# Performance work log

Hardware: AMD Instinct MI355X
Metric: run time of the kernel (lower is better)

## Reference

```python
import jax, jax.numpy as jnp
import numpy as np

EPS = 1e-05


def reference(inputs, c1, h1, c2, h2, w, b, norm_w, norm_b):
    B = inputs.shape[0]
    U = inputs.shape[1]
    # [B, 3U] @ [3U, 5U] + [1, 5U]
    x = jnp.concatenate([inputs, h1, h2], axis=1)
    res = x @ w + b
    # split into 5 contiguous gates -> [B, 5, U], layer-norm each gate over last axis
    g = res.reshape(B, 5, U)
    m = jnp.mean(g, axis=-1, keepdims=True)
    v = jnp.var(g, axis=-1, keepdims=True)  # biased variance, matches tf.nn.moments
    ln = (g - m) / jnp.sqrt(v + EPS) * norm_w[None, :, :] + norm_b[None, :, :]
    i, j, f, f2, o = ln[:, 0], ln[:, 1], ln[:, 2], ln[:, 3], ln[:, 4]
    new_c = c1 * jax.nn.sigmoid(f) + c2 * jax.nn.sigmoid(f2) + jax.nn.sigmoid(i) * jnp.tanh(j)
    new_h = new_c * jax.nn.sigmoid(o)
    return new_c, new_h


def setup_inputs() -> dict:
    B, U = 16384, 512
    key = jax.random.key(0)
    ks = jax.random.split(key, 6)
    return {
        "inputs": jax.random.normal(ks[0], (B, U), dtype=jnp.float32),
        "c1": jax.random.normal(ks[1], (B, U), dtype=jnp.float32),
        "h1": jax.random.normal(ks[2], (B, U), dtype=jnp.float32),
        "c2": jax.random.normal(ks[3], (B, U), dtype=jnp.float32),
        "h2": jax.random.normal(ks[4], (B, U), dtype=jnp.float32),
        "w": jax.random.normal(ks[5], (3 * U, 5 * U), dtype=jnp.float32) * (1.0 / np.sqrt(3 * U)),
        "b": jnp.zeros((1, 5 * U), dtype=jnp.float32),
        "norm_w": jnp.ones((5, U), dtype=jnp.float32),
        "norm_b": jnp.zeros((5, U), dtype=jnp.float32),
    }
```

## Files before the change

kernel.cpp:

```cpp
#include <hip/hip_runtime.h>
#include <hip/hip_bf16.h>
#include <cstdint>

#define B_DIM 16384
#define U_DIM 512
#define K_DIM 1536
#define N_DIM 2560
#define NT    24

typedef unsigned short u16;
typedef __attribute__((ext_vector_type(4))) unsigned short u16x4;
typedef __attribute__((ext_vector_type(8))) unsigned short u16x8;
typedef __attribute__((ext_vector_type(8))) short bf16x8;
typedef __attribute__((ext_vector_type(4))) float f32x4;

__device__ __forceinline__ u16 f2bf(float f) {
    uint32_t u = __builtin_bit_cast(uint32_t, f);
    u += 0x7FFFu + ((u >> 16) & 1u);
    return (u16)(u >> 16);
}
__device__ __forceinline__ float bf2f(u16 h) {
    uint32_t u = ((uint32_t)h) << 16;
    return __builtin_bit_cast(float, u);
}

__global__ void __launch_bounds__(256) cvt_x_kernel(
    const float* __restrict__ inp, const float* __restrict__ h1,
    const float* __restrict__ h2, u16* __restrict__ xb)
{
    int idx = blockIdx.x * 256 + threadIdx.x;
    const int total4 = B_DIM * K_DIM / 4;
    if (idx >= total4) return;
    int e = idx * 4;
    int b = e / K_DIM;
    int k = e - b * K_DIM;
    const float* src;
    if (k < 512)       src = inp + b * 512 + k;
    else if (k < 1024) src = h1  + b * 512 + (k - 512);
    else               src = h2  + b * 512 + (k - 1024);
    float4 v = *(const float4*)src;
    u16x4 o;
    o.x = f2bf(v.x); o.y = f2bf(v.y); o.z = f2bf(v.z); o.w = f2bf(v.w);
    *(u16x4*)(xb + e) = o;
}

__global__ void __launch_bounds__(256) cvt_wT_kernel(
    const float* __restrict__ w, u16* __restrict__ wT)
{
    __shared__ float tile[32][33];
    const int n0 = blockIdx.x * 32;
    const int k0 = blockIdx.y * 32;
    const int tx = threadIdx.x & 31;
    const int ty = threadIdx.x >> 5;
#pragma unroll
    for (int i = 0; i < 4; ++i) {
        int kk = ty + i * 8;
        tile[kk][tx] = w[(k0 + kk) * N_DIM + n0 + tx];
    }
    __syncthreads();
#pragma unroll
    for (int i = 0; i < 4; ++i) {
        int nn = ty + i * 8;
        wT[(int64_t)(n0 + nn) * K_DIM + k0 + tx] = f2bf(tile[tx][nn]);
    }
}

__device__ __forceinline__ void gload_lds16(const void* g, void* l) {
    __builtin_amdgcn_global_load_lds(
        (const __attribute__((address_space(1))) void*)g,
        (__attribute__((address_space(3))) void*)l, 16, 0, 0);
}

#define BAR    __builtin_amdgcn_s_barrier()
#define FENCE  asm volatile("" ::: "memory")
#define VMCNT3 asm volatile("s_waitcnt vmcnt(3)" ::: "memory")
#define LGKM0  do { asm volatile("s_waitcnt lgkmcnt(0)" ::: "memory"); \
                    __builtin_amdgcn_sched_barrier(0); } while (0)

__global__ void __launch_bounds__(512, 2) gemm_kernel(
    const u16* __restrict__ A, const u16* __restrict__ Bt,
    u16* __restrict__ C)
{
    __shared__ u16 sm[49152];

    const int tid  = threadIdx.x;
    const int lane = tid & 63;
    const int wave = tid >> 6;

    int bid = blockIdx.x;
    int swz = (bid & 7) * 160 + (bid >> 3);
    const int bm = (swz / 10) * 128;
    const int bn = (swz % 10) * 256;

    const int wm = (wave >> 2) * 64;
    const int wn = (wave & 3) * 64;

    const int l15 = lane & 15, cq = lane >> 4;
    const int s   = (((l15 & 1) << 2) | cq) ^ ((l15 >> 1) & 7);
    const int rdA = ((wm + l15) >> 1) * 64 + s * 8;
    const int rdB = ((wn + l15) >> 1) * 64 + s * 8;

    const int line0 = tid >> 3;
    const int rc    = (tid & 7) ^ (line0 & 7);
    const int srow  = line0 * 2 + (rc >> 2);
    const int sc8   = (rc & 3) * 8;
    const u16* gA = A  + (int64_t)(bm + srow) * K_DIM + sc8;
    const u16* gB = Bt + (int64_t)(bn + srow) * K_DIM + sc8;
    char* ldA = (char*)sm + tid * 16;
    char* ldB = (char*)sm + 16384 + tid * 16;

#define STAGE(ks, kt, buf) do {                                            \
        const u16* ga_ = gA + (kt) + (ks) * 32;                            \
        const u16* gb_ = gB + (kt) + (ks) * 32;                            \
        char* la_ = ldA + (buf) * 49152 + (ks) * 8192;                     \
        char* lb_ = ldB + (buf) * 49152 + (ks) * 16384;                    \
        gload_lds16(ga_, la_);                                             \
        gload_lds16(gb_, lb_);                                             \
        gload_lds16(gb_ + 128 * K_DIM, lb_ + 8192);                        \
    } while (0)

    f32x4 acc[4][4];
#pragma unroll
    for (int i = 0; i < 4; ++i)
#pragma unroll
        for (int j = 0; j < 4; ++j) acc[i][j] = (f32x4)(0.0f);

    STAGE(0, 0, 0);
    STAGE(1, 0, 0);
    VMCNT3;
    BAR; FENCE;

    bf16x8 af[4], bfr[4];

#define LOAD_A4(BASE) _Pragma("unroll")                                    \
    for (int mi = 0; mi < 4; ++mi) af[mi] = *(const bf16x8*)((BASE) + mi * 512)
#define LOAD_B4(BASE) _Pragma("unroll")                                    \
    for (int n = 0; n < 4; ++n) bfr[n] = *(const bf16x8*)((BASE) + n * 512)
#define MFMA16 _Pragma("unroll")                                           \
    for (int mi = 0; mi < 4; ++mi) { _Pragma("unroll")                     \
        for (int n = 0; n < 4; ++n)                                        \
            acc[mi][n] = __builtin_amdgcn_mfma_f32_16x16x32_bf16(          \
                af[mi], bfr[n], acc[mi][n], 0, 0, 0); }

    for (int t = 0; t < NT; ++t) {
        const int cur = t & 1, nxt = cur ^ 1;
        const int ktn = ((t + 1) == NT) ? 0 : (t + 1) * 64;
        const u16* base = sm + cur * 24576;

        LOAD_A4(base + rdA);
        LOAD_B4(base + 8192 + rdB);
        STAGE(0, ktn, nxt);
        BAR; LGKM0;
        __builtin_amdgcn_s_setprio(1);
        MFMA16;
        __builtin_amdgcn_s_setprio(0);
        VMCNT3;
        BAR; FENCE;

        LOAD_A4(base + 4096 + rdA);
        LOAD_B4(base + 8192 + 8192 + rdB);
        STAGE(1, ktn, nxt);
        BAR; LGKM0;
        __builtin_amdgcn_s_setprio(1);
        MFMA16;
        __builtin_amdgcn_s_setprio(0);
        VMCNT3;
        BAR; FENCE;
    }

    const int ecol = lane & 15;
    const int erow = (lane >> 4) * 4;
#pragma unroll
    for (int m = 0; m < 4; ++m)
#pragma unroll
        for (int n = 0; n < 4; ++n)
#pragma unroll
            for (int r = 0; r < 4; ++r) {
                int grow = bm + wm + m * 16 + erow + r;
                int gcol = bn + wn + n * 16 + ecol;
                C[(int64_t)grow * N_DIM + gcol] = f2bf(acc[m][n][r]);
            }
}

__device__ __forceinline__ float fsig(float x) {
    return 1.0f / (1.0f + __expf(-x));
}
__device__ __forceinline__ float ftanh(float x) {
    float e = __expf(-2.0f * fabsf(x));
    float r = (1.0f - e) / (1.0f + e);
    return copysignf(r, x);
}

__global__ void __launch_bounds__(256) ln_pointwise_kernel(
    const u16*  __restrict__ res,  const float* __restrict__ bias,
    const float* __restrict__ c1,  const float* __restrict__ c2,
    const float* __restrict__ nw,  const float* __restrict__ nb,
    float* __restrict__ out)
{
    const int wave = threadIdx.x >> 6;
    const int lane = threadIdx.x & 63;
    const int b    = blockIdx.x * 4 + wave;
    const u16* row = res + (int64_t)b * N_DIM;
    const int u0 = lane * 8;

    float v[5][8];
    float rstd[5], mean[5];

#pragma unroll
    for (int g = 0; g < 5; ++g) {
        u16x8 raw = *(const u16x8*)(row + g * 512 + u0);
        const float4* bp = (const float4*)(bias + g * 512 + u0);
        float4 b0 = bp[0], b1 = bp[1];
        v[g][0] = bf2f(raw[0]) + b0.x;  v[g][1] = bf2f(raw[1]) + b0.y;
        v[g][2] = bf2f(raw[2]) + b0.z;  v[g][3] = bf2f(raw[3]) + b0.w;
        v[g][4] = bf2f(raw[4]) + b1.x;  v[g][5] = bf2f(raw[5]) + b1.y;
        v[g][6] = bf2f(raw[6]) + b1.z;  v[g][7] = bf2f(raw[7]) + b1.w;
        float s = 0.f, q = 0.f;
#pragma unroll
        for (int j = 0; j < 8; ++j) { s += v[g][j]; q += v[g][j] * v[g][j]; }
#pragma unroll
        for (int off = 1; off < 64; off <<= 1) {
            s += __shfl_xor(s, off);
            q += __shfl_xor(q, off);
        }
        float m   = s * (1.0f / 512.0f);
        float var = q * (1.0f / 512.0f) - m * m;
        mean[g] = m;
        rstd[g] = rsqrtf(var + 1e-5f);
    }

#pragma unroll
    for (int g = 0; g < 5; ++g) {
        const float4* wp = (const float4*)(nw + g * 512 + u0);
        const float4* bp = (const float4*)(nb + g * 512 + u0);
        float4 w0 = wp[0], w1 = wp[1], n0 = bp[0], n1 = bp[1];
        float ws[8] = {w0.x, w0.y, w0.z, w0.w, w1.x, w1.y, w1.z, w1.w};
        float ns[8] = {n0.x, n0.y, n0.z, n0.w, n1.x, n1.y, n1.z, n1.w};
#pragma unroll
        for (int j = 0; j < 8; ++j)
            v[g][j] = (v[g][j] - mean[g]) * rstd[g] * ws[j] + ns[j];
    }

    const float4* c1p = (const float4*)(c1 + (int64_t)b * 512 + u0);
    const float4* c2p = (const float4*)(c2 + (int64_t)b * 512 + u0);
    float4 c1a = c1p[0], c1b = c1p[1], c2a = c2p[0], c2b = c2p[1];
    float c1s[8] = {c1a.x, c1a.y, c1a.z, c1a.w, c1b.x, c1b.y, c1b.z, c1b.w};
    float c2s[8] = {c2a.x, c2a.y, c2a.z, c2a.w, c2b.x, c2b.y, c2b.z, c2b.w};

    float oc[8], oh[8];
#pragma unroll
    for (int j = 0; j < 8; ++j) {
        float ig  = fsig(v[0][j]);
        float jg  = ftanh(v[1][j]);
        float fg  = fsig(v[2][j]);
        float f2g = fsig(v[3][j]);
        float og  = fsig(v[4][j]);
        float cc  = c1s[j] * fg + c2s[j] * f2g + ig * jg;
        oc[j] = cc;
        oh[j] = cc * og;
    }

    float* oC = out + (int64_t)b * 512 + u0;
    float* oH = out + (int64_t)B_DIM * U_DIM + (int64_t)b * 512 + u0;
    ((float4*)oC)[0] = make_float4(oc[0], oc[1], oc[2], oc[3]);
    ((float4*)oC)[1] = make_float4(oc[4], oc[5], oc[6], oc[7]);
    ((float4*)oH)[0] = make_float4(oh[0], oh[1], oh[2], oh[3]);
    ((float4*)oH)[1] = make_float4(oh[4], oh[5], oh[6], oh[7]);
}

extern "C" void kernel_launch(void* const* d_in, const int* in_sizes, int n_in,
                              void* d_out, int out_size, void* d_ws, size_t ws_size,
                              hipStream_t stream)
{
    const float* inputs = (const float*)d_in[0];
    const float* c1     = (const float*)d_in[1];
    const float* h1     = (const float*)d_in[2];
    const float* c2     = (const float*)d_in[3];
    const float* h2     = (const float*)d_in[4];
    const float* w      = (const float*)d_in[5];
    const float* bias   = (const float*)d_in[6];
    const float* nw     = (const float*)d_in[7];
    const float* nb     = (const float*)d_in[8];
    float* out = (float*)d_out;

    const size_t XB_BYTES = (size_t)B_DIM * K_DIM * 2;
    const size_t WT_BYTES = (size_t)N_DIM * K_DIM * 2;
    u16* xb  = (u16*)d_ws;
    u16* wT  = (u16*)((char*)d_ws + XB_BYTES);
    u16* res = (u16*)((char*)d_ws + XB_BYTES + WT_BYTES);

    cvt_x_kernel<<<(B_DIM * K_DIM / 4 + 255) / 256, 256, 0, stream>>>(inputs, h1, h2, xb);
    cvt_wT_kernel<<<dim3(N_DIM / 32, K_DIM / 32), 256, 0, stream>>>(w, wT);
    gemm_kernel<<<(B_DIM / 128) * (N_DIM / 256), 512, 0, stream>>>(xb, wT, res);
    ln_pointwise_kernel<<<B_DIM / 4, 256, 0, stream>>>(res, bias, c1, c2, nw, nb, out);
}
```

Measured before the change: 383.1 us.

## Enlarge GEMM tile to 256x256 and load B fragments directly into registers

```diff
diff --git a/kernel.cpp b/kernel.cpp
--- a/kernel.cpp
+++ b/kernel.cpp
@@ -73,105 +73,120 @@
 
 #define BAR    __builtin_amdgcn_s_barrier()
 #define FENCE  asm volatile("" ::: "memory")
-#define VMCNT3 asm volatile("s_waitcnt vmcnt(3)" ::: "memory")
-#define LGKM0  do { asm volatile("s_waitcnt lgkmcnt(0)" ::: "memory"); \
-                    __builtin_amdgcn_sched_barrier(0); } while (0)
+#define VMCNT8 asm volatile("s_waitcnt vmcnt(8)" ::: "memory")
 
 __global__ void __launch_bounds__(512, 2) gemm_kernel(
     const u16* __restrict__ A, const u16* __restrict__ Bt,
     u16* __restrict__ C)
 {
-    __shared__ u16 sm[49152];
+    __shared__ u16 sm[2][16384];
 
     const int tid  = threadIdx.x;
     const int lane = tid & 63;
     const int wave = tid >> 6;
 
     int bid = blockIdx.x;
-    int swz = (bid & 7) * 160 + (bid >> 3);
-    const int bm = (swz / 10) * 128;
+    int swz = (bid & 7) * 80 + (bid >> 3);
+    const int bm = (swz / 10) * 256;
     const int bn = (swz % 10) * 256;
 
-    const int wm = (wave >> 2) * 64;
+    const int wm = (wave >> 2) * 128;
     const int wn = (wave & 3) * 64;
 
     const int l15 = lane & 15, cq = lane >> 4;
     const int s   = (((l15 & 1) << 2) | cq) ^ ((l15 >> 1) & 7);
-    const int rdA = ((wm + l15) >> 1) * 64 + s * 8;
-    const int rdB = ((wn + l15) >> 1) * 64 + s * 8;
-
-    const int line0 = tid >> 3;
-    const int rc    = (tid & 7) ^ (line0 & 7);
-    const int srow  = line0 * 2 + (rc >> 2);
-    const int sc8   = (rc & 3) * 8;
-    const u16* gA = A  + (int64_t)(bm + srow) * K_DIM + sc8;
-    const u16* gB = Bt + (int64_t)(bn + srow) * K_DIM + sc8;
-    char* ldA = (char*)sm + tid * 16;
-    char* ldB = (char*)sm + 16384 + tid * 16;
-
-#define STAGE(ks, kt, buf) do {                                            \
-        const u16* ga_ = gA + (kt) + (ks) * 32;                            \
-        const u16* gb_ = gB + (kt) + (ks) * 32;                            \
-        char* la_ = ldA + (buf) * 49152 + (ks) * 8192;                     \
-        char* lb_ = ldB + (buf) * 49152 + (ks) * 16384;                    \
-        gload_lds16(ga_, la_);                                             \
-        gload_lds16(gb_, lb_);                                             \
-        gload_lds16(gb_ + 128 * K_DIM, lb_ + 8192);                        \
+    const int rdA = ((wm >> 1) + (l15 >> 1)) * 64 + s * 8;
+
+    const int lineJ0 = (wave * 2 + 0) * 8 + (lane >> 3);
+    const int lineJ1 = (wave * 2 + 1) * 8 + (lane >> 3);
+    const int rc0 = (lane & 7) ^ (lineJ0 & 7);
+    const int rc1 = (lane & 7) ^ (lineJ1 & 7);
+    const int srow0 = lineJ0 * 2 + (rc0 >> 2), sc0 = (rc0 & 3) * 8;
+    const int srow1 = lineJ1 * 2 + (rc1 >> 2), sc1 = (rc1 & 3) * 8;
+    const u16* gA0 = A + (int64_t)(bm + srow0) * K_DIM + sc0;
+    const u16* gA1 = A + (int64_t)(bm + srow1) * K_DIM + sc1;
+    char* ldA0 = (char*)&sm[0][0] + (wave * 2 + 0) * 1024 + lane * 16;
+    char* ldA1 = (char*)&sm[0][0] + (wave * 2 + 1) * 1024 + lane * 16;
+
+#define STAGE(KT, BUF) do {                                                \
+        gload_lds16(gA0 + (KT),      ldA0 + (BUF) * 32768);                \
+        gload_lds16(gA1 + (KT),      ldA1 + (BUF) * 32768);                \
+        gload_lds16(gA0 + (KT) + 32, ldA0 + (BUF) * 32768 + 16384);        \
+        gload_lds16(gA1 + (KT) + 32, ldA1 + (BUF) * 32768 + 16384);        \
     } while (0)
 
-    f32x4 acc[4][4];
-#pragma unroll
-    for (int i = 0; i < 4; ++i)
+    const u16* gBf = Bt + (int64_t)(bn + wn + l15) * K_DIM + cq * 8;
+
+#define LOADB(BB, KT) do {                                                 \
+        _Pragma("unroll")                                                  \
+        for (int ks = 0; ks < 2; ++ks) {                                   \
+            _Pragma("unroll")                                              \
+            for (int n = 0; n < 4; ++n)                                    \
+                BB[ks * 4 + n] = *(const bf16x8*)(gBf +                    \
+                    n * (16 * K_DIM) + (KT) + ks * 32);                    \
+        }                                                                  \
+    } while (0)
+
+    f32x4 acc[8][4];
+#pragma unroll
+    for (int i = 0; i < 8; ++i)
 #pragma unroll
         for (int j = 0; j < 4; ++j) acc[i][j] = (f32x4)(0.0f);
 
-    STAGE(0, 0, 0);
-    STAGE(1, 0, 0);
-    VMCNT3;
+    bf16x8 bb0[8], bb1[8];
+
+#define MFMA16(MB, BB, KS) do {                                            \
+        __builtin_amdgcn_s_setprio(1);                                     \
+        _Pragma("unroll")                                                  \
+        for (int mi = 0; mi < 4; ++mi) { _Pragma("unroll")                 \
+            for (int n = 0; n < 4; ++n)                                    \
+                acc[(MB) + mi][n] = __builtin_amdgcn_mfma_f32_16x16x32_bf16( \
+                    af[mi], BB[(KS) * 4 + n], acc[(MB) + mi][n], 0, 0, 0); } \
+        __builtin_amdgcn_s_setprio(0);                                     \
+    } while (0)
+
+#define COMPUTE(BUF, BB) do {                                              \
+        _Pragma("unroll")                                                  \
+        for (int ks = 0; ks < 2; ++ks) {                                   \
+            const u16* ab = &sm[BUF][0] + ks * 8192 + rdA;                 \
+            bf16x8 af[4];                                                  \
+            _Pragma("unroll")                                              \
+            for (int mi = 0; mi < 4; ++mi)                                 \
+                af[mi] = *(const bf16x8*)(ab + mi * 512);                  \
+            MFMA16(0, BB, ks);                                             \
+            _Pragma("unroll")                                              \
+            for (int mi = 0; mi < 4; ++mi)                                 \
+                af[mi] = *(const bf16x8*)(ab + (4 + mi) * 512);            \
+            MFMA16(4, BB, ks);                                             \
+        }                                                                  \
+    } while (0)
+
+    STAGE(0, 0);
+    LOADB(bb0, 0);
+    VMCNT8;
     BAR; FENCE;
 
-    bf16x8 af[4], bfr[4];
-
-#define LOAD_A4(BASE) _Pragma("unroll")                                    \
-    for (int mi = 0; mi < 4; ++mi) af[mi] = *(const bf16x8*)((BASE) + mi * 512)
-#define LOAD_B4(BASE) _Pragma("unroll")                                    \
-    for (int n = 0; n < 4; ++n) bfr[n] = *(const bf16x8*)((BASE) + n * 512)
-#define MFMA16 _Pragma("unroll")                                           \
-    for (int mi = 0; mi < 4; ++mi) { _Pragma("unroll")                     \
-        for (int n = 0; n < 4; ++n)                                        \
-            acc[mi][n] = __builtin_amdgcn_mfma_f32_16x16x32_bf16(          \
-                af[mi], bfr[n], acc[mi][n], 0, 0, 0); }
-
-    for (int t = 0; t < NT; ++t) {
-        const int cur = t & 1, nxt = cur ^ 1;
-        const int ktn = ((t + 1) == NT) ? 0 : (t + 1) * 64;
-        const u16* base = sm + cur * 24576;
-
-        LOAD_A4(base + rdA);
-        LOAD_B4(base + 8192 + rdB);
-        STAGE(0, ktn, nxt);
-        BAR; LGKM0;
-        __builtin_amdgcn_s_setprio(1);
-        MFMA16;
-        __builtin_amdgcn_s_setprio(0);
-        VMCNT3;
-        BAR; FENCE;
-
-        LOAD_A4(base + 4096 + rdA);
-        LOAD_B4(base + 8192 + 8192 + rdB);
-        STAGE(1, ktn, nxt);
-        BAR; LGKM0;
-        __builtin_amdgcn_s_setprio(1);
-        MFMA16;
-        __builtin_amdgcn_s_setprio(0);
-        VMCNT3;
-        BAR; FENCE;
+    for (int t2 = 0; t2 < NT; t2 += 2) {
+        {
+            const int ktn = (t2 + 1) * 64;
+            STAGE(ktn, 1);
+            LOADB(bb1, ktn);
+            COMPUTE(0, bb0);
+            VMCNT8; BAR; FENCE;
+        }
+        {
+            const int ktn = (t2 + 2 == NT) ? 0 : (t2 + 2) * 64;
+            STAGE(ktn, 0);
+            LOADB(bb0, ktn);
+            COMPUTE(1, bb1);
+            VMCNT8; BAR; FENCE;
+        }
     }
 
     const int ecol = lane & 15;
     const int erow = (lane >> 4) * 4;
 #pragma unroll
-    for (int m = 0; m < 4; ++m)
+    for (int m = 0; m < 8; ++m)
 #pragma unroll
         for (int n = 0; n < 4; ++n)
 #pragma unroll
@@ -215,15 +230,15 @@
         v[g][2] = bf2f(raw[2]) + b0.z;  v[g][3] = bf2f(raw[3]) + b0.w;
         v[g][4] = bf2f(raw[4]) + b1.x;  v[g][5] = bf2f(raw[5]) + b1.y;
         v[g][6] = bf2f(raw[6]) + b1.z;  v[g][7] = bf2f(raw[7]) + b1.w;
-        float s = 0.f, q = 0.f;
-#pragma unroll
-        for (int j = 0; j < 8; ++j) { s += v[g][j]; q += v[g][j] * v[g][j]; }
+        float ss = 0.f, q = 0.f;
+#pragma unroll
+        for (int j = 0; j < 8; ++j) { ss += v[g][j]; q += v[g][j] * v[g][j]; }
 #pragma unroll
         for (int off = 1; off < 64; off <<= 1) {
-            s += __shfl_xor(s, off);
-            q += __shfl_xor(q, off);
+            ss += __shfl_xor(ss, off);
+            q  += __shfl_xor(q, off);
         }
-        float m   = s * (1.0f / 512.0f);
+        float m   = ss * (1.0f / 512.0f);
         float var = q * (1.0f / 512.0f) - m * m;
         mean[g] = m;
         rstd[g] = rsqrtf(var + 1e-5f);
@@ -291,6 +306,6 @@
 
     cvt_x_kernel<<<(B_DIM * K_DIM / 4 + 255) / 256, 256, 0, stream>>>(inputs, h1, h2, xb);
     cvt_wT_kernel<<<dim3(N_DIM / 32, K_DIM / 32), 256, 0, stream>>>(w, wT);
-    gemm_kernel<<<(B_DIM / 128) * (N_DIM / 256), 512, 0, stream>>>(xb, wT, res);
+    gemm_kernel<<<(B_DIM / 256) * (N_DIM / 256), 512, 0, stream>>>(xb, wT, res);
     ln_pointwise_kernel<<<B_DIM / 4, 256, 0, stream>>>(res, bias, c1, c2, nw, nb, out);
 }
```

Result: slower. 457.5 us (+19.4%).
